# Kernel optimization log

Hardware: AMD Instinct MI355X
Metric: run time of the kernel (lower is better)

## Reference

```python
import jax, jax.numpy as jnp
import numpy as np

B, T, D, H, O = 128, 512, 128, 256, 1


def setup_inputs() -> dict:
    key = jax.random.key(0)
    ks = jax.random.split(key, 11)
    s = lambda n: 1.0 / np.sqrt(H)
    u = lambda k, shape: jax.random.uniform(k, shape, jnp.float32, -s(0), s(0))
    return {
        "X": jax.random.normal(ks[0], (B, T, D), jnp.float32),
        "Wih0": u(ks[1], (4 * H, D)),
        "Whh0": u(ks[2], (4 * H, H)),
        "bih0": u(ks[3], (4 * H,)),
        "bhh0": u(ks[4], (4 * H,)),
        "Wih1": u(ks[5], (4 * H, H)),
        "Whh1": u(ks[6], (4 * H, H)),
        "bih1": u(ks[7], (4 * H,)),
        "bhh1": u(ks[8], (4 * H,)),
        "Wfc": u(ks[9], (O, H)),
        "bfc": u(ks[10], (O,)),
    }


def _lstm_layer(x, Wih, Whh, bih, bhh):
    # x: [B, T, Din] -> h sequence [B, T, H]
    # Precompute input contributions for all timesteps (one big GEMM).
    xg = jnp.einsum("btd,gd->btg", x, Wih) + bih + bhh  # [B, T, 4H]
    xg = jnp.transpose(xg, (1, 0, 2))  # [T, B, 4H]
    h0 = jnp.zeros((x.shape[0], Whh.shape[1]), x.dtype)
    c0 = jnp.zeros_like(h0)

    def step(carry, xt):
        h, c = carry
        gates = xt + h @ Whh.T  # [B, 4H]
        i, f, g, o = jnp.split(gates, 4, axis=-1)  # PyTorch gate order i,f,g,o
        i = jax.nn.sigmoid(i)
        f = jax.nn.sigmoid(f)
        g = jnp.tanh(g)
        o = jax.nn.sigmoid(o)
        c = f * c + i * g
        h = o * jnp.tanh(c)
        return (h, c), h

    (_, _), hs = jax.lax.scan(step, (h0, c0), xg)
    return jnp.transpose(hs, (1, 0, 2))  # [B, T, H]


def reference(X, Wih0, Whh0, bih0, bhh0, Wih1, Whh1, bih1, bhh1, Wfc, bfc):
    h1 = _lstm_layer(X, Wih0, Whh0, bih0, bhh0)
    h2 = _lstm_layer(h1, Wih1, Whh1, bih1, bhh1)
    return h2[:, -1, :] @ Wfc.T + bfc  # [B, O]
```

## Files before the change

kernel.cpp:

```cpp
#include <hip/hip_runtime.h>

typedef unsigned short u16;
typedef unsigned int u32;
typedef __attribute__((ext_vector_type(8))) short bf8;
typedef __attribute__((ext_vector_type(4))) float f4;

#define DEVI static __device__ __forceinline__

constexpr int Bb = 128, Tt = 512, Dd = 128, Hh = 256, G4 = 1024;
constexpr int CH  = 32;
constexpr int NCH = Tt / CH;
constexpr int MCH = CH * Bb;
constexpr size_t CHF = (size_t)MCH * G4;

DEVI u16 f2bf(float f) {
  union { float f; u32 u; } v; v.f = f;
  u32 r = v.u + 0x7FFFu + ((v.u >> 16) & 1u);
  return (u16)(r >> 16);
}
DEVI float bf2f(u16 b) { union { u32 u; float f; } v; v.u = ((u32)b) << 16; return v.f; }
DEVI float frcp(float x) { return __builtin_amdgcn_rcpf(x); }
DEVI float sigm(float x) { return frcp(1.f + __expf(-x)); }
DEVI float tanh_f(float x) { return 1.f - 2.f * frcp(1.f + __expf(2.f * x)); }
DEVI f4 mfma16(bf8 a, bf8 b, f4 c) {
  return __builtin_amdgcn_mfma_f32_16x16x32_bf16(a, b, c, 0, 0, 0);
}

DEVI u32 ld_u32_coh(const u32* p) {
  u32 r;
  asm volatile("global_load_dword %0, %1, off sc0 sc1\ns_waitcnt vmcnt(0)"
               : "=&v"(r) : "v"(p) : "memory");
  return r;
}
DEVI bf8 ld16_coh(const u16* p) {
  bf8 r;
  asm volatile("global_load_dwordx4 %0, %1, off sc0 sc1" : "=&v"(r) : "v"(p) : "memory");
  return r;
}
DEVI void st16_coh(u16* p, bf8 v) {
  asm volatile("global_store_dwordx4 %0, %1, off sc0 sc1" :: "v"(p), "v"(v) : "memory");
}
DEVI void st_u32_coh(u32* p, u32 v) {
  asm volatile("global_store_dword %0, %1, off sc0 sc1" :: "v"(p), "v"(v) : "memory");
}


__global__ void k_prep_x(const float* __restrict__ X, u16* __restrict__ Xhi, u16* __restrict__ Xlo) {
  size_t idx = (size_t)blockIdx.x * 256 + threadIdx.x;
  int d = (int)(idx % Dd);
  size_t bt = idx / Dd;
  int b = (int)(bt / Tt), t = (int)(bt % Tt);
  float x = X[idx];
  u16 hi = f2bf(x);
  u16 lo = f2bf(x - bf2f(hi));
  size_t o = ((size_t)t * Bb + b) * Dd + d;
  Xhi[o] = hi; Xlo[o] = lo;
}

__global__ void k_split(const float* __restrict__ W, u16* __restrict__ hi_, u16* __restrict__ lo_) {
  size_t idx = (size_t)blockIdx.x * 256 + threadIdx.x;
  float v = W[idx];
  u16 hi = f2bf(v);
  hi_[idx] = hi;
  lo_[idx] = f2bf(v - bf2f(hi));
}

__global__ void k_prep_whh(const float* __restrict__ Whh, u16* __restrict__ W2) {
  int idx = blockIdx.x * 256 + threadIdx.x;
  int i = idx & 7, lane = (idx >> 3) & 63, kt = (idx >> 9) & 7, jtg = idx >> 12;
  int jp = (jtg << 4) + (lane & 15);
  int k  = ((lane >> 4) << 3) + i + (kt << 5);
  W2[idx] = f2bf(Whh[(size_t)jp * Hh + k]);
}

__global__ void k_bias(const float* __restrict__ a, const float* __restrict__ b, float* __restrict__ o) {
  int i = blockIdx.x * 256 + threadIdx.x;
  if (i < G4) o[i] = a[i] + b[i];
}

__global__ void k_init(u32* __restrict__ tags) {
  int i = blockIdx.x * 256 + threadIdx.x;
  if (i < 2 * (Tt + 1) * 64) {
    int row = (i >> 6) % (Tt + 1);
    tags[i] = (row == 0) ? 1u : 0u;
  }
}

__global__ void k_zrow(u16* __restrict__ a, u16* __restrict__ b) {
  int i = blockIdx.x * 256 + threadIdx.x;
  if (i < Bb * Hh) { a[i] = 0; b[i] = 0; }
}

template <int K, bool ALO>
DEVI void gemm_body(char* smem, const u16* __restrict__ Ahi, const u16* __restrict__ Alo,
                    const u16* __restrict__ Whi, const u16* __restrict__ Wlo,
                    const float* __restrict__ bias, float* __restrict__ Cout,
                    int bx, int by) {
  u16* AsH = (u16*)smem;
  u16* AsL = (u16*)(smem + 8192);
  const int tid = threadIdx.x, l = tid & 63;
  const int w = tid >> 6, wm = w >> 1, wn = w & 1;
  const int lrow = l & 15, lk = (l >> 4) << 3;
  const size_t m0 = (size_t)bx * 128;
  const int n0 = by * 128;

  f4 acc[4][4];
  size_t colK[4];
#pragma unroll
  for (int ni = 0; ni < 4; ++ni) {
    int col = n0 + wn * 64 + ni * 16 + lrow;
    float bv = bias[col];
    colK[ni] = (size_t)col * K + lk;
#pragma unroll
    for (int mi = 0; mi < 4; ++mi) {
      acc[mi][ni][0] = bv; acc[mi][ni][1] = bv; acc[mi][ni][2] = bv; acc[mi][ni][3] = bv;
    }
  }

  for (int kk = 0; kk < K; kk += 32) {
    __syncthreads();
#pragma unroll
    for (int s = 0; s < 2; ++s) {
      int slot = s * 256 + tid;
      int r = slot >> 2, kg = (slot & 3) << 3;
      *(bf8*)&AsH[r * 32 + kg] = *(const bf8*)&Ahi[(m0 + r) * K + kk + kg];
      if constexpr (ALO) *(bf8*)&AsL[r * 32 + kg] = *(const bf8*)&Alo[(m0 + r) * K + kk + kg];
    }
    __syncthreads();

    bf8 bh[4], bl[4];
#pragma unroll
    for (int ni = 0; ni < 4; ++ni) {
      bh[ni] = *(const bf8*)&Whi[colK[ni] + kk];
      bl[ni] = *(const bf8*)&Wlo[colK[ni] + kk];
    }
    bf8 ah[4], al[4];
#pragma unroll
    for (int mi = 0; mi < 4; ++mi) {
      ah[mi] = *(const bf8*)&AsH[(wm * 64 + mi * 16 + lrow) * 32 + lk];
      if constexpr (ALO) al[mi] = *(const bf8*)&AsL[(wm * 64 + mi * 16 + lrow) * 32 + lk];
    }
#pragma unroll
    for (int mi = 0; mi < 4; ++mi)
#pragma unroll
      for (int ni = 0; ni < 4; ++ni) {
        acc[mi][ni] = mfma16(ah[mi], bh[ni], acc[mi][ni]);
        acc[mi][ni] = mfma16(ah[mi], bl[ni], acc[mi][ni]);
        if constexpr (ALO) acc[mi][ni] = mfma16(al[mi], bh[ni], acc[mi][ni]);
      }
  }

  f4* C4 = (f4*)Cout;
#pragma unroll
  for (int mi = 0; mi < 4; ++mi) {
    int gg = wm * 4 + mi;
#pragma unroll
    for (int ni = 0; ni < 4; ++ni) {
      int colb = by * 128 + wn * 64 + ni * 16;
      int q  = colb >> 8;
      int ss = (colb >> 5) & 7;
      int wt = (colb >> 4) & 1;
      C4[(((((size_t)bx * 8 + gg) * 8 + ss) * 2 + wt) * 4 + q) * 64 + l] = acc[mi][ni];
    }
  }
}

DEVI void recur_body(char* smem, const float* __restrict__ xg, const u16* __restrict__ W2,
                     u16* h, float* cst, u32* tags,
                     int t0, int role, int sub) {
  u16* wlds = (u16*)smem;
  u16* sbuf = (u16*)(smem + 65536);
  const int tid = threadIdx.x, l = tid & 63, w = tid >> 6;
  const int lrow = l & 15, lg = l >> 4;
  const int g = sub & 7, s = sub >> 3;
  const int b_base = g << 4;
  const int w1 = w & 1;

  for (int u = 0; u < 16; ++u) {
    int f = u * 256 + tid;
    int jl = f >> 9, kt = (f >> 6) & 7, e = f & 63;
    int jtg = ((jl >> 1) << 4) + (s << 1) + (jl & 1);
    *(bf8*)&wlds[f << 3] = *(const bf8*)&W2[((size_t)jtg << 12) + (kt << 9) + (e << 3)];
  }

  const int jmy = (s << 5) + (w1 << 4) + lrow;
  float cc4[4] = {0.f, 0.f, 0.f, 0.f};
  if (tid < 128 && t0 > 0) {
#pragma unroll
    for (int rr = 0; rr < 4; ++rr)
      cc4[rr] = cst[(size_t)(b_base + (lg << 2) + rr) * Hh + jmy];
  }
  __syncthreads();

  const f4* xb = (const f4*)xg + ((((size_t)g * 8 + s) * 2 + w1) * 4) * 64 + l;
  f4 xgn[4];
  if (tid < 128) {
#pragma unroll
    for (int q = 0; q < 4; ++q) xgn[q] = xb[q << 6];
  }

  for (int t = 0; t < CH; ++t) {
    const int T = t0 + t;
    if (tid < 128) {
      const u32 tagv = (u32)(T + 1);
      u32* tp = tags + ((((size_t)role * (Tt + 1) + T) * 8 + g) << 3) + (tid & 7);
      const u16* hr = h + ((size_t)(role ? (T & 1) : T) * Bb + b_base + lrow) * Hh + (lg << 3);

      int seen = (ld_u32_coh(tp) == tagv);
      bf8 af[8];
#pragma unroll
      for (int kt = 0; kt < 8; ++kt) af[kt] = ld16_coh(hr + (kt << 5));
      if (!__all(seen)) {
        int it = 0;
        do { seen = (ld_u32_coh(tp) == tagv); } while (!__all(seen) && ++it < (1 << 20));
#pragma unroll
        for (int kt = 0; kt < 8; ++kt) af[kt] = ld16_coh(hr + (kt << 5));
      }
      __builtin_amdgcn_sched_barrier(0);

      f4 acc[4];
#pragma unroll
      for (int q = 0; q < 4; ++q) acc[q] = xgn[q];

      bf8 bcur[4], bnxt[4];
#pragma unroll
      for (int q = 0; q < 4; ++q)
        bcur[q] = *(const bf8*)&wlds[((((q << 1) | w1) << 3) << 9) + (l << 3)];
#pragma unroll
      for (int kt = 0; kt < 8; ++kt) {
        if (kt < 7) {
#pragma unroll
          for (int q = 0; q < 4; ++q)
            bnxt[q] = *(const bf8*)&wlds[(((((q << 1) | w1) << 3) | (kt + 1)) << 9) + (l << 3)];
        }
        asm volatile("s_waitcnt vmcnt(%0)" :: "i"(7 - kt) : "memory");
        __builtin_amdgcn_sched_barrier(0);
#pragma unroll
        for (int q = 0; q < 4; ++q) acc[q] = mfma16(af[kt], bcur[q], acc[q]);
#pragma unroll
        for (int q = 0; q < 4; ++q) bcur[q] = bnxt[q];
      }

      u16 hv[4];
#pragma unroll
      for (int rr = 0; rr < 4; ++rr) {
        float gi = sigm(acc[0][rr]);
        float gf = sigm(acc[1][rr]);
        float gg = tanh_f(acc[2][rr]);
        float go = sigm(acc[3][rr]);
        float c2 = gf * cc4[rr] + gi * gg;
        cc4[rr] = c2;
        hv[rr] = f2bf(go * tanh_f(c2));
      }
#pragma unroll
      for (int rr = 0; rr < 4; ++rr)
        sbuf[(((lg << 2) + rr) << 5) + (w1 << 4) + lrow] = hv[rr];
    }
    __syncthreads();
    if (tid < 64) {
      int b = tid >> 2, gg = tid & 3;
      bf8 v = *(const bf8*)&sbuf[(b << 5) + (gg << 3)];
      u16* hw = h + ((size_t)(role ? ((T + 1) & 1) : (T + 1)) * Bb + b_base + b) * Hh
                + (s << 5) + (gg << 3);
      st16_coh(hw, v);
      asm volatile("s_waitcnt vmcnt(0)" ::: "memory");
      if (tid == 0) {
        u32* tq = tags + ((((size_t)role * (Tt + 1) + T + 1) * 8 + g) << 3) + s;
        st_u32_coh(tq, (u32)(T + 2));
      }
    }
    if (tid < 128 && t + 1 < CH) {
#pragma unroll
      for (int q = 0; q < 4; ++q) xgn[q] = xb[(size_t)(t + 1) * 32768 + (q << 6)];
    }
  }

  if (tid < 128) {
#pragma unroll
    for (int rr = 0; rr < 4; ++rr)
      cst[(size_t)(b_base + (lg << 2) + rr) * Hh + jmy] = cc4[rr];
  }
}

__global__ void __launch_bounds__(256) k_mega(
    const u16* gAh, const u16* gAl,
    const u16* W0h, const u16* W0l, const float* b0,
    const u16* gBa,
    const u16* W1h, const u16* W1l, const float* b1,
    float* xgAw, const float* xgAr,
    float* xgBw, const float* xgBr,
    const u16* W2a, const u16* W2b,
    u16* h1, u16* h2r, float* cstA, float* cstB,
    u32* tags, int d) {
  __shared__ __align__(16) char smem[66560];
  const int bid = blockIdx.x;
  if (bid < 128) {
    const int role = bid >> 6;
    if (role == 0) {
      if (d < 1 || d > NCH) return;
      recur_body(smem, xgAr, W2a, h1, cstA, tags, (d - 1) * CH, 0, bid & 63);
    } else {
      if (d < 3 || d > NCH + 2) return;
      recur_body(smem, xgBr, W2b, h2r, cstB, tags, (d - 3) * CH, 1, bid & 63);
    }
  } else if (bid < 384) {
    if (d > NCH - 1) return;
    int q = bid - 128;
    gemm_body<Dd, true>(smem, gAh, gAl, W0h, W0l, b0, xgAw, q & 31, q >> 5);
  } else {
    if (d < 2 || d > NCH + 1) return;
    int q = bid - 384;
    gemm_body<Hh, false>(smem, gBa, nullptr, W1h, W1l, b1, xgBw, q & 31, q >> 5);
  }
}

__global__ void k_fc(const u16* __restrict__ h2l, const float* __restrict__ Wfc,
                     const float* __restrict__ bfc, float* __restrict__ out) {
  int b = threadIdx.x;
  if (b < Bb) {
    float s = bfc[0];
    for (int j = 0; j < Hh; ++j) s += bf2f(h2l[(size_t)b * Hh + j]) * Wfc[j];
    out[b] = s;
  }
}

extern "C" void kernel_launch(void* const* d_in, const int* in_sizes, int n_in,
                              void* d_out, int out_size, void* d_ws, size_t ws_size,
                              hipStream_t stream) {
  const float* X    = (const float*)d_in[0];
  const float* Wih0 = (const float*)d_in[1];
  const float* Whh0 = (const float*)d_in[2];
  const float* bih0 = (const float*)d_in[3];
  const float* bhh0 = (const float*)d_in[4];
  const float* Wih1 = (const float*)d_in[5];
  const float* Whh1 = (const float*)d_in[6];
  const float* bih1 = (const float*)d_in[7];
  const float* bhh1 = (const float*)d_in[8];
  const float* Wfc  = (const float*)d_in[9];
  const float* bfc  = (const float*)d_in[10];

  char* base = (char*)d_ws;
  size_t off = 0;
  auto alloc = [&](size_t bytes) -> char* {
    char* p = base + off;
    off = (off + bytes + 255) & ~(size_t)255;
    return p;
  };

  u16* Xhi = (u16*)alloc((size_t)Bb * Tt * Dd * 2);
  u16* Xlo = (u16*)alloc((size_t)Bb * Tt * Dd * 2);
  u16* W0h = (u16*)alloc((size_t)G4 * Dd * 2);
  u16* W0l = (u16*)alloc((size_t)G4 * Dd * 2);
  u16* W1h = (u16*)alloc((size_t)G4 * Hh * 2);
  u16* W1l = (u16*)alloc((size_t)G4 * Hh * 2);
  u16* W2a = (u16*)alloc((size_t)G4 * Hh * 2);
  u16* W2b = (u16*)alloc((size_t)G4 * Hh * 2);
  float* b0 = (float*)alloc(G4 * 4);
  float* b1 = (float*)alloc(G4 * 4);
  float* xgA = (float*)alloc((size_t)2 * CHF * 4);
  float* xgB = (float*)alloc((size_t)2 * CHF * 4);
  u16* h1Z = (u16*)alloc((size_t)(Tt + 1) * Bb * Hh * 2);
  u16* h2r = (u16*)alloc((size_t)2 * Bb * Hh * 2);
  float* cstA = (float*)alloc((size_t)Bb * Hh * 4);
  float* cstB = (float*)alloc((size_t)Bb * Hh * 4);
  u32* tags = (u32*)alloc((size_t)2 * (Tt + 1) * 64 * 4);

  k_init<<<(2 * (Tt + 1) * 64 + 255) / 256, 256, 0, stream>>>(tags);
  k_zrow<<<(Bb * Hh + 255) / 256, 256, 0, stream>>>(h1Z, h2r);
  k_prep_x<<<(Bb * Tt * Dd) / 256, 256, 0, stream>>>(X, Xhi, Xlo);
  k_split<<<(G4 * Dd) / 256, 256, 0, stream>>>(Wih0, W0h, W0l);
  k_split<<<(G4 * Hh) / 256, 256, 0, stream>>>(Wih1, W1h, W1l);
  k_prep_whh<<<(G4 * Hh) / 256, 256, 0, stream>>>(Whh0, W2a);
  k_prep_whh<<<(G4 * Hh) / 256, 256, 0, stream>>>(Whh1, W2b);
  k_bias<<<4, 256, 0, stream>>>(bih0, bhh0, b0);
  k_bias<<<4, 256, 0, stream>>>(bih1, bhh1, b1);

  for (int dd = 0; dd <= NCH + 2; ++dd) {
    int ca = dd < NCH ? dd : NCH - 1;
    int cb = dd < 2 ? 0 : (dd - 2 < NCH ? dd - 2 : NCH - 1);
    k_mega<<<640, 256, 0, stream>>>(
        Xhi + (size_t)ca * MCH * Dd, Xlo + (size_t)ca * MCH * Dd,
        W0h, W0l, b0,
        h1Z + ((size_t)(cb * CH) + 1) * Bb * Hh,
        W1h, W1l, b1,
        xgA + (size_t)(dd & 1) * CHF, xgA + (size_t)((dd + 1) & 1) * CHF,
        xgB + (size_t)(dd & 1) * CHF, xgB + (size_t)((dd + 1) & 1) * CHF,
        W2a, W2b, h1Z, h2r, cstA, cstB, tags, dd);
  }
  k_fc<<<1, 128, 0, stream>>>(h2r, Wfc, bfc, (float*)d_out);

  (void)in_sizes; (void)n_in; (void)out_size; (void)ws_size;
}
```

Measured before the change: 1.551 ms.

## Pipeline recurrent h stores on a separate wave with double-buffered LDS

Moves the global store of each timestep's hidden state and its ready-tag publish from the compute waves to a separate wave (threads 128-191). That wave writes step t-1's results while the compute waves work on step t, using a double-buffered LDS staging area. The next step's input-gate loads are now issued right after the MFMA loop via inline asm, and the block barrier becomes a raw s_barrier. The aim is to take store latency and the vmcnt(0) wait off the recurrence critical path. The cost is one extra loop iteration and a one-step delay in publishing h, which other blocks that depend on it will see later.

Measured after the change: 1.803 ms. +16.2%, slower.

```diff
diff --git a/kernel.cpp b/kernel.cpp
--- a/kernel.cpp
+++ b/kernel.cpp
@@ -42,6 +42,11 @@
 }
 DEVI void st_u32_coh(u32* p, u32 v) {
   asm volatile("global_store_dword %0, %1, off sc0 sc1" :: "v"(p), "v"(v) : "memory");
+}
+DEVI f4 ld16f(const float* p) {
+  f4 r;
+  asm volatile("global_load_dwordx4 %0, %1, off" : "=&v"(r) : "v"(p) : "memory");
+  return r;
 }
 
 
@@ -196,12 +201,13 @@
   f4 xgn[4];
   if (tid < 128) {
 #pragma unroll
-    for (int q = 0; q < 4; ++q) xgn[q] = xb[q << 6];
-  }
-
-  for (int t = 0; t < CH; ++t) {
+    for (int q = 0; q < 4; ++q) xgn[q] = ld16f((const float*)(xb + (q << 6)));
+  }
+
+  for (int t = 0; t <= CH; ++t) {
     const int T = t0 + t;
-    if (tid < 128) {
+
+    if (tid < 128 && t < CH) {
       const u32 tagv = (u32)(T + 1);
       u32* tp = tags + ((((size_t)role * (Tt + 1) + T) * 8 + g) << 3) + (tid & 7);
       const u16* hr = h + ((size_t)(role ? (T & 1) : T) * Bb + b_base + lrow) * Hh + (lg << 3);
@@ -239,6 +245,12 @@
         for (int q = 0; q < 4; ++q) acc[q] = mfma16(af[kt], bcur[q], acc[q]);
 #pragma unroll
         for (int q = 0; q < 4; ++q) bcur[q] = bnxt[q];
+      }
+
+      if (t + 1 < CH) {
+#pragma unroll
+        for (int q = 0; q < 4; ++q)
+          xgn[q] = ld16f((const float*)(xb + (size_t)(t + 1) * 32768 + (q << 6)));
       }
 
       u16 hv[4];
@@ -254,25 +266,19 @@
       }
 #pragma unroll
       for (int rr = 0; rr < 4; ++rr)
-        sbuf[(((lg << 2) + rr) << 5) + (w1 << 4) + lrow] = hv[rr];
-    }
-    __syncthreads();
-    if (tid < 64) {
-      int b = tid >> 2, gg = tid & 3;
-      bf8 v = *(const bf8*)&sbuf[(b << 5) + (gg << 3)];
-      u16* hw = h + ((size_t)(role ? ((T + 1) & 1) : (T + 1)) * Bb + b_base + b) * Hh
+        sbuf[((t & 1) << 9) + (((lg << 2) + rr) << 5) + (w1 << 4) + lrow] = hv[rr];
+    } else if (tid >= 128 && tid < 192 && t > 0) {
+      int u = tid - 128;
+      int b = u >> 2, gg = u & 3;
+      bf8 v = *(const bf8*)&sbuf[(((t - 1) & 1) << 9) + (b << 5) + (gg << 3)];
+      u16* hw = h + ((size_t)(role ? (T & 1) : T) * Bb + b_base + b) * Hh
                 + (s << 5) + (gg << 3);
       st16_coh(hw, v);
       asm volatile("s_waitcnt vmcnt(0)" ::: "memory");
-      if (tid == 0) {
-        u32* tq = tags + ((((size_t)role * (Tt + 1) + T + 1) * 8 + g) << 3) + s;
-        st_u32_coh(tq, (u32)(T + 2));
-      }
-    }
-    if (tid < 128 && t + 1 < CH) {
-#pragma unroll
-      for (int q = 0; q < 4; ++q) xgn[q] = xb[(size_t)(t + 1) * 32768 + (q << 6)];
-    }
+      if (u == 0)
+        st_u32_coh(tags + ((((size_t)role * (Tt + 1) + T) * 8 + g) << 3) + s, (u32)(T + 1));
+    }
+    asm volatile("s_waitcnt lgkmcnt(0)\ns_barrier" ::: "memory");
   }
 
   if (tid < 128) {
@@ -292,7 +298,7 @@
     const u16* W2a, const u16* W2b,
     u16* h1, u16* h2r, float* cstA, float* cstB,
     u32* tags, int d) {
-  __shared__ __align__(16) char smem[66560];
+  __shared__ __align__(16) char smem[67584];
   const int bid = blockIdx.x;
   if (bid < 128) {
     const int role = bid >> 6;
@@ -381,7 +387,7 @@
     k_mega<<<640, 256, 0, stream>>>(
         Xhi + (size_t)ca * MCH * Dd, Xlo + (size_t)ca * MCH * Dd,
         W0h, W0l, b0,
-        h1Z + ((size_t)(cb * CH) + 1) * Bb * Hh,
+        h1Z + (size_t)(cb * CH + 1) * Bb * Hh,
         W1h, W1l, b1,
         xgA + (size_t)(dd & 1) * CHF, xgA + (size_t)((dd + 1) & 1) * CHF,
         xgB + (size_t)(dd & 1) * CHF, xgB + (size_t)((dd + 1) & 1) * CHF,
```
